# Kernel optimization log

Hardware: AMD Instinct MI355X
Metric: run time of the kernel (lower is better)

The kernel has to match this reference:

```python
import jax, jax.numpy as jnp
import numpy as np


def _chamfer(xyz1, xyz2):
    # xyz1: [B,N,3], xyz2: [B,M,3]
    sq1 = jnp.sum(xyz1 * xyz1, axis=-1)               # [B,N]
    sq2 = jnp.sum(xyz2 * xyz2, axis=-1)               # [B,M]
    cross = jnp.einsum('bnc,bmc->bnm', xyz1, xyz2)    # [B,N,M]
    d = sq1[:, :, None] + sq2[:, None, :] - 2.0 * cross  # [B,N,M] squared dists
    dist1 = jnp.min(d, axis=2)                        # [B,N]
    idx1 = jnp.argmin(d, axis=2).astype(jnp.int32)    # [B,N]
    dist2 = jnp.min(d, axis=1)                        # [B,M]
    idx2 = jnp.argmin(d, axis=1).astype(jnp.int32)    # [B,M]
    return dist1, dist2, idx1, idx2


def setup_inputs() -> dict:
    key = jax.random.key(0)
    k1, k2 = jax.random.split(key)
    B, N, M = 2, 8192, 8192
    xyz1 = jax.random.normal(k1, (B, N, 3), dtype=jnp.float32)
    xyz2 = jax.random.normal(k2, (B, M, 3), dtype=jnp.float32)
    return {"xyz1": xyz1, "xyz2": xyz2}


def reference(xyz1, xyz2):
    # Matches ChamferDistanceFunction.forward: returns (dist1, dist2, idx1, idx2)
    # with SQUARED distances, as in the CUDA kernel.
    return _chamfer(xyz1, xyz2)
```

## Files before the change

kernel.cpp:

```cpp
#include <hip/hip_runtime.h>
#include <stdint.h>

#define TPB   256
#define Q     4
#define CHUNK 128

typedef unsigned long long ull;

__device__ __forceinline__ uint32_t enc_f32(float f) {
    uint32_t u = __float_as_uint(f);
    return (u & 0x80000000u) ? ~u : (u | 0x80000000u);
}

__device__ __forceinline__ float sq_np(float x, float y, float z) {
    return __fadd_rn(__fadd_rn(__fmul_rn(x, x), __fmul_rn(y, y)), __fmul_rn(z, z));
}

__global__ void __launch_bounds__(TPB) chamfer_pass1(
    const float* __restrict__ xyz1, const float* __restrict__ xyz2,
    ull* __restrict__ P, int B, int N, int M)
{
    __shared__ float4 pts[CHUNK];

    int z   = blockIdx.z;
    int dir = z / B;
    int b   = z - dir * B;

    const float* src; const float* dst; int Ns, Nd; size_t ebase;
    if (dir == 0) { src = xyz1; dst = xyz2; Ns = N; Nd = M; ebase = (size_t)b * N; }
    else          { src = xyz2; dst = xyz1; Ns = M; Nd = N; ebase = (size_t)B * N + (size_t)b * M; }

    int t     = threadIdx.x;
    int mbase = blockIdx.y * CHUNK;

    for (int i = t; i < CHUNK; i += TPB) {
        int m = mbase + i;
        if (m < Nd) {
            const float* p = dst + ((size_t)b * Nd + m) * 3;
            float x = p[0], y = p[1], zz = p[2];
            pts[i] = make_float4(x, y, zz, sq_np(x, y, zz));
        } else {
            pts[i] = make_float4(0.f, 0.f, 0.f, 3.0e38f);
        }
    }

    int n0 = blockIdx.x * (TPB * Q) + t;
    float qx[Q], qy[Q], qz[Q], qs[Q];
    #pragma unroll
    for (int k = 0; k < Q; ++k) {
        int n = n0 + k * TPB;
        if (n < Ns) {
            const float* p = src + ((size_t)b * Ns + n) * 3;
            qx[k] = p[0]; qy[k] = p[1]; qz[k] = p[2];
            qs[k] = sq_np(qx[k], qy[k], qz[k]);
        } else { qx[k] = 0.f; qy[k] = 0.f; qz[k] = 0.f; qs[k] = 0.f; }
    }
    __syncthreads();

    float best[Q];
    int   bidx[Q];
    #pragma unroll
    for (int k = 0; k < Q; ++k) { best[k] = 3.4e38f; bidx[k] = 0; }

    #pragma unroll 4
    for (int i = 0; i < CHUNK; ++i) {
        float4 q = pts[i];
        #pragma unroll
        for (int k = 0; k < Q; ++k) {
            float cross = __fadd_rn(__fadd_rn(__fmul_rn(qx[k], q.x), __fmul_rn(qy[k], q.y)),
                                    __fmul_rn(qz[k], q.z));
            float s = __fadd_rn(qs[k], q.w);
            float d = fmaf(-2.0f, cross, s);
            if (d < best[k]) { best[k] = d; bidx[k] = mbase + i; }
        }
    }

    #pragma unroll
    for (int k = 0; k < Q; ++k) {
        int n = n0 + k * TPB;
        if (n < Ns) {
            ull packed = ((ull)enc_f32(best[k]) << 32) | (unsigned int)bidx[k];
            atomicMin(&P[ebase + n], packed);
        }
    }
}

__global__ void __launch_bounds__(256) chamfer_unpack(
    const ull* __restrict__ P, float* __restrict__ out, int entries)
{
    int e = blockIdx.x * 256 + threadIdx.x;
    if (e < entries) {
        ull pk = P[e];
        uint32_t encu = (uint32_t)(pk >> 32);
        uint32_t idx  = (uint32_t)pk;
        uint32_t bits = (encu & 0x80000000u) ? (encu & 0x7FFFFFFFu) : ~encu;
        out[e]           = __uint_as_float(bits);
        out[entries + e] = (float)idx;
    }
}

__global__ void __launch_bounds__(1024) chamfer_unpack_inplace(float* __restrict__ out)
{
    const int entries = 32768;
    const ull* P = (const ull*)out;
    int t = threadIdx.x;
    ull v[32];
    #pragma unroll
    for (int k = 0; k < 32; ++k) v[k] = P[t + k * 1024];
    __syncthreads();
    #pragma unroll
    for (int k = 0; k < 32; ++k) {
        int e = t + k * 1024;
        ull pk = v[k];
        uint32_t encu = (uint32_t)(pk >> 32);
        uint32_t idx  = (uint32_t)pk;
        uint32_t bits = (encu & 0x80000000u) ? (encu & 0x7FFFFFFFu) : ~encu;
        out[e]           = __uint_as_float(bits);
        out[entries + e] = (float)idx;
    }
}

extern "C" void kernel_launch(void* const* d_in, const int* in_sizes, int n_in,
                              void* d_out, int out_size, void* d_ws, size_t ws_size,
                              hipStream_t stream) {
    const float* xyz1 = (const float*)d_in[0];
    const float* xyz2 = (const float*)d_in[1];
    const int B = 2;
    const int N = in_sizes[0] / (B * 3);
    const int M = in_sizes[1] / (B * 3);

    float* out = (float*)d_out;
    const int entries = B * N + B * M;
    const size_t pbytes = (size_t)entries * sizeof(ull);

    int maxP = (N > M) ? N : M;
    dim3 grid((maxP + TPB * Q - 1) / (TPB * Q), (maxP + CHUNK - 1) / CHUNK, 2 * B);

    if (ws_size >= pbytes) {
        ull* P = (ull*)d_ws;
        hipMemsetAsync(d_ws, 0xFF, pbytes, stream);
        chamfer_pass1<<<grid, TPB, 0, stream>>>(xyz1, xyz2, P, B, N, M);
        chamfer_unpack<<<(entries + 255) / 256, 256, 0, stream>>>(P, out, entries);
    } else {
        ull* P = (ull*)d_out;
        hipMemsetAsync(d_out, 0xFF, pbytes, stream);
        chamfer_pass1<<<grid, TPB, 0, stream>>>(xyz1, xyz2, P, B, N, M);
        if (entries == 32768) {
            chamfer_unpack_inplace<<<1, 1024, 0, stream>>>(out);
        } else {
            chamfer_unpack<<<1, 1, 0, stream>>>((const ull*)d_out, out, 0);
        }
    }
}
```

Before: 111.6 us.

## Fuse pass1 and unpack with last-block counter and persistent device buffer

Replaces the memset, pass1 and unpack launches with a single fused kernel. Per-point packed minima live in a device-global buffer, and a per-column counter identifies the last y-block to arrive, which unpacks the results and resets the entries to all-ones. This removes the per-call memset and the separate unpack launch. In exchange, state persists across calls, the code depends on the counter and reset logic being correct, and each block now pays a threadfence and a counter atomic.

```diff
diff --git a/kernel.cpp b/kernel.cpp
--- a/kernel.cpp
+++ b/kernel.cpp
@@ -4,8 +4,13 @@
 #define TPB   256
 #define Q     4
 #define CHUNK 128
+#define MAXE  32768
+#define MAXG  256
 
 typedef unsigned long long ull;
+
+__device__ ull g_P[MAXE];
+__device__ ull g_cnt[MAXG] = {};
 
 __device__ __forceinline__ uint32_t enc_f32(float f) {
     uint32_t u = __float_as_uint(f);
@@ -16,11 +21,20 @@
     return __fadd_rn(__fadd_rn(__fmul_rn(x, x), __fmul_rn(y, y)), __fmul_rn(z, z));
 }
 
-__global__ void __launch_bounds__(TPB) chamfer_pass1(
+__device__ __forceinline__ void unpack1(ull pk, float* __restrict__ out, int entries, int e) {
+    uint32_t encu = (uint32_t)(pk >> 32);
+    uint32_t idx  = (uint32_t)pk;
+    uint32_t bits = (encu & 0x80000000u) ? (encu & 0x7FFFFFFFu) : ~encu;
+    out[e]           = __uint_as_float(bits);
+    out[entries + e] = (float)idx;
+}
+
+__global__ void __launch_bounds__(TPB) chamfer_fused(
     const float* __restrict__ xyz1, const float* __restrict__ xyz2,
-    ull* __restrict__ P, int B, int N, int M)
+    float* __restrict__ out, int B, int N, int M)
 {
     __shared__ float4 pts[CHUNK];
+    __shared__ int s_last;
 
     int z   = blockIdx.z;
     int dir = z / B;
@@ -80,6 +94,102 @@
         int n = n0 + k * TPB;
         if (n < Ns) {
             ull packed = ((ull)enc_f32(best[k]) << 32) | (unsigned int)bidx[k];
+            atomicMin(&g_P[ebase + n], packed);
+        }
+    }
+
+    __threadfence();
+    __syncthreads();
+    if (t == 0) {
+        int cidx = blockIdx.z * gridDim.x + blockIdx.x;
+        ull old = __hip_atomic_fetch_add(&g_cnt[cidx], 1ull,
+                                         __ATOMIC_ACQ_REL, __HIP_MEMORY_SCOPE_AGENT);
+        s_last = (old == (ull)(gridDim.y - 1)) ? 1 : 0;
+        if (s_last)
+            __hip_atomic_store(&g_cnt[cidx], 0ull,
+                               __ATOMIC_RELAXED, __HIP_MEMORY_SCOPE_AGENT);
+    }
+    __syncthreads();
+    if (s_last) {
+        __threadfence();
+        const int entries = B * (N + M);
+        #pragma unroll
+        for (int k = 0; k < Q; ++k) {
+            int n = n0 + k * TPB;
+            if (n < Ns) {
+                int e = (int)ebase + n;
+                ull pk = __hip_atomic_load(&g_P[e], __ATOMIC_RELAXED, __HIP_MEMORY_SCOPE_AGENT);
+                __hip_atomic_store(&g_P[e], ~0ull, __ATOMIC_RELAXED, __HIP_MEMORY_SCOPE_AGENT);
+                unpack1(pk, out, entries, e);
+            }
+        }
+    }
+}
+
+__global__ void __launch_bounds__(TPB) chamfer_pass1(
+    const float* __restrict__ xyz1, const float* __restrict__ xyz2,
+    ull* __restrict__ P, int B, int N, int M)
+{
+    __shared__ float4 pts[CHUNK];
+
+    int z   = blockIdx.z;
+    int dir = z / B;
+    int b   = z - dir * B;
+
+    const float* src; const float* dst; int Ns, Nd; size_t ebase;
+    if (dir == 0) { src = xyz1; dst = xyz2; Ns = N; Nd = M; ebase = (size_t)b * N; }
+    else          { src = xyz2; dst = xyz1; Ns = M; Nd = N; ebase = (size_t)B * N + (size_t)b * M; }
+
+    int t     = threadIdx.x;
+    int mbase = blockIdx.y * CHUNK;
+
+    for (int i = t; i < CHUNK; i += TPB) {
+        int m = mbase + i;
+        if (m < Nd) {
+            const float* p = dst + ((size_t)b * Nd + m) * 3;
+            float x = p[0], y = p[1], zz = p[2];
+            pts[i] = make_float4(x, y, zz, sq_np(x, y, zz));
+        } else {
+            pts[i] = make_float4(0.f, 0.f, 0.f, 3.0e38f);
+        }
+    }
+
+    int n0 = blockIdx.x * (TPB * Q) + t;
+    float qx[Q], qy[Q], qz[Q], qs[Q];
+    #pragma unroll
+    for (int k = 0; k < Q; ++k) {
+        int n = n0 + k * TPB;
+        if (n < Ns) {
+            const float* p = src + ((size_t)b * Ns + n) * 3;
+            qx[k] = p[0]; qy[k] = p[1]; qz[k] = p[2];
+            qs[k] = sq_np(qx[k], qy[k], qz[k]);
+        } else { qx[k] = 0.f; qy[k] = 0.f; qz[k] = 0.f; qs[k] = 0.f; }
+    }
+    __syncthreads();
+
+    float best[Q];
+    int   bidx[Q];
+    #pragma unroll
+    for (int k = 0; k < Q; ++k) { best[k] = 3.4e38f; bidx[k] = 0; }
+
+    #pragma unroll 4
+    for (int i = 0; i < CHUNK; ++i) {
+        float4 q = pts[i];
+        #pragma unroll
+        for (int k = 0; k < Q; ++k) {
+            float cross = __fadd_rn(__fadd_rn(__fmul_rn(qx[k], q.x), __fmul_rn(qy[k], q.y)),
+                                    __fmul_rn(qz[k], q.z));
+            float s = __fadd_rn(qs[k], q.w);
+            float d = fmaf(-2.0f, cross, s);
+            if (d < best[k]) { best[k] = d; bidx[k] = mbase + i; }
+        }
+    }
+
+    #pragma unroll
+    for (int k = 0; k < Q; ++k) {
+        int n = n0 + k * TPB;
+        if (n < Ns) {
+            ull packed = ((ull)enc_f32(best[k]) << 32) | (unsigned int)bidx[k];
             atomicMin(&P[ebase + n], packed);
         }
     }
@@ -134,7 +244,28 @@
     const size_t pbytes = (size_t)entries * sizeof(ull);
 
     int maxP = (N > M) ? N : M;
-    dim3 grid((maxP + TPB * Q - 1) / (TPB * Q), (maxP + CHUNK - 1) / CHUNK, 2 * B);
+    int gx = (maxP + TPB * Q - 1) / (TPB * Q);
+    int yc = (maxP + CHUNK - 1) / CHUNK;
+    int zc = 2 * B;
+    dim3 grid(gx, yc, zc);
+
+    if (entries <= MAXE && gx * zc <= MAXG) {
+        static void* pP = nullptr;
+        static int   sym_tried = 0;
+        static int   inited = 0;
+        if (!sym_tried) {
+            sym_tried = 1;
+            if (hipGetSymbolAddress(&pP, HIP_SYMBOL(g_P)) != hipSuccess) pP = nullptr;
+        }
+        if (pP) {
+            if (!inited) {
+                hipMemsetAsync(pP, 0xFF, (size_t)MAXE * sizeof(ull), stream);
+                inited = 1;
+            }
+            chamfer_fused<<<grid, TPB, 0, stream>>>(xyz1, xyz2, out, B, N, M);
+            return;
+        }
+    }
 
     if (ws_size >= pbytes) {
         ull* P = (ull*)d_ws;
```

Result: slower. 229.5 us (+105.5%).
